# Optimization experiments

Measured on AMD Instinct MI355X. Metric: run time of the kernel, lower is better.

## Reference

```python
import jax, jax.numpy as jnp
import numpy as np

N_NODES = 100000
N_EDGES = 1600000
D_IN = 256
D_OUT = 256


def setup_inputs() -> dict:
    key = jax.random.key(0)
    ks = jax.random.split(key, 6)
    x_src = jax.random.normal(ks[0], (N_NODES, D_IN), dtype=jnp.float32)
    x_tgt = jax.random.normal(ks[1], (N_NODES, D_IN), dtype=jnp.float32)
    edge_index = jax.random.randint(ks[2], (2, N_EDGES), 0, N_NODES, dtype=jnp.int64)
    # torch Linear stores weight [out, in]; we store transposed [in, out] (same math)
    W_l = jax.random.normal(ks[3], (D_IN, D_OUT), dtype=jnp.float32) / np.sqrt(D_IN)
    b_l = jax.random.normal(ks[4], (D_OUT,), dtype=jnp.float32) * 0.01
    W_r = jax.random.normal(ks[5], (D_IN, D_OUT), dtype=jnp.float32) / np.sqrt(D_IN)
    return {"x_src": x_src, "x_tgt": x_tgt, "edge_index": edge_index,
            "W_l": W_l, "b_l": b_l, "W_r": W_r}


def reference(x_src, x_tgt, edge_index, W_l, b_l, W_r):
    row, col = edge_index[0], edge_index[1]
    n_tgt = x_tgt.shape[0]
    # gather source features along edges, scatter-mean into target nodes
    msgs = x_src[row]                                               # [E, D_IN]
    sums = jax.ops.segment_sum(msgs, col, num_segments=n_tgt)        # [N_tgt, D_IN]
    cnt = jax.ops.segment_sum(jnp.ones((row.shape[0],), x_src.dtype), col,
                              num_segments=n_tgt)                    # [N_tgt]
    aggr = sums / jnp.maximum(cnt, 1.0)[:, None]                     # mean; empty segs -> 0
    return aggr @ W_l + b_l + x_tgt @ W_r
```

## Files before the change

### kernel.cpp

```cpp
#include <hip/hip_runtime.h>
#include <hip/hip_bf16.h>

#define D 256
#define BW 128
#define CH 16384
#define SBCAP 2560

typedef __attribute__((ext_vector_type(8))) short short8;
typedef __attribute__((ext_vector_type(4))) float floatx4;
typedef __attribute__((ext_vector_type(4))) int intx4;

static __device__ __forceinline__ unsigned short f2bf(float f) {
  unsigned int u = __builtin_bit_cast(unsigned int, f);
  u += 0x7FFFu + ((u >> 16) & 1u);
  return (unsigned short)(u >> 16);
}

static __device__ __forceinline__ void gld_lds16(const unsigned short* g, unsigned short* l) {
  __builtin_amdgcn_global_load_lds(
      (const __attribute__((address_space(1))) unsigned int*)g,
      (__attribute__((address_space(3))) unsigned int*)l, 16, 0, 0);
}

static __device__ __forceinline__ int detect_is64(const int* ei32, int* sflag) {
  if (threadIdx.x < 64) {
    int v = ei32[2 * threadIdx.x + 1];
    unsigned long long nz = __ballot(v != 0);
    if (threadIdx.x == 0) *sflag = (nz == 0ULL) ? 1 : 0;
  }
  __syncthreads();
  return *sflag;
}

static __device__ __forceinline__ int edge_at(const void* ei, int is64, long long idx) {
  return is64 ? (int)((const long long*)ei)[idx] : ((const int*)ei)[idx];
}

__global__ __launch_bounds__(256) void scatter_kernel(const void* __restrict__ ei,
                                                      unsigned int* __restrict__ bucketbuf,
                                                      int* __restrict__ bcur,
                                                      int E, int N, int NBUCK) {
  __shared__ unsigned int recs[CH];
  __shared__ unsigned short bkt[CH];
  __shared__ unsigned short inv[CH];
  __shared__ int cnt[1025];
  __shared__ int lofs[1025];
  __shared__ int gb[1024];
  __shared__ int sflag;
  int t = threadIdx.x;
  long long base = (long long)blockIdx.x * CH;
  if (base >= E) return;
  int is64 = detect_is64((const int*)ei, &sflag);
  int count = (int)((E - base) < CH ? (E - base) : CH);

  for (int i = t; i <= NBUCK; i += 256) cnt[i] = 0;
  __syncthreads();

  for (int i = t; i < count; i += 256) {
    int c = edge_at(ei, is64, (long long)E + base + i);
    int s = edge_at(ei, is64, base + i);
    bool valid = (unsigned)c < (unsigned)N && (unsigned)s < (unsigned)N;
    int b = valid ? (c >> 7) : NBUCK;
    recs[i] = valid ? (((unsigned)s << 7) | (unsigned)(c & (BW - 1))) : 0u;
    bkt[i] = (unsigned short)b;
    atomicAdd(&cnt[b], 1);
  }
  __syncthreads();

  int i0 = t * 4;
  int v0 = (i0 + 0 <= NBUCK) ? cnt[i0 + 0] : 0;
  int v1 = (i0 + 1 <= NBUCK) ? cnt[i0 + 1] : 0;
  int v2 = (i0 + 2 <= NBUCK) ? cnt[i0 + 2] : 0;
  int v3 = (i0 + 3 <= NBUCK) ? cnt[i0 + 3] : 0;
  gb[t] = v0 + v1 + v2 + v3;
  __syncthreads();
  for (int d = 1; d < 256; d <<= 1) {
    int v = (t >= d) ? gb[t - d] : 0;
    __syncthreads();
    gb[t] += v;
    __syncthreads();
  }
  int excl = (t == 0) ? 0 : gb[t - 1];
  __syncthreads();
  if (i0 + 0 <= NBUCK) lofs[i0 + 0] = excl;
  if (i0 + 1 <= NBUCK) lofs[i0 + 1] = excl + v0;
  if (i0 + 2 <= NBUCK) lofs[i0 + 2] = excl + v0 + v1;
  if (i0 + 3 <= NBUCK) lofs[i0 + 3] = excl + v0 + v1 + v2;
  __syncthreads();

#pragma unroll
  for (int j = 0; j < 4; ++j) {
    int idx = i0 + j;
    if (idx < NBUCK) {
      int len = lofs[idx + 1] - lofs[idx];
      gb[idx] = (len > 0) ? atomicAdd(&bcur[idx], len) : 0;
    }
  }
  for (int i = t; i <= NBUCK; i += 256) cnt[i] = lofs[i];
  __syncthreads();

  for (int i = t; i < count; i += 256) {
    int p = atomicAdd(&cnt[bkt[i]], 1);
    inv[p] = (unsigned short)i;
  }
  __syncthreads();

  for (int p = t; p < count; p += 256) {
    int i = inv[p];
    int b = bkt[i];
    if (b < NBUCK) {
      int pos = gb[b] + (p - lofs[b]);
      if (pos < SBCAP) bucketbuf[(size_t)b * SBCAP + pos] = recs[i];
    }
  }
}

__global__ void bucket_scan_kernel(const int* __restrict__ bcur, int* __restrict__ bucket_base,
                                   int* __restrict__ offsets, int NBUCK, int N) {
  __shared__ int part[1024];
  int t = threadIdx.x;
  int tot = 0;
  if (t < NBUCK) {
    int v = bcur[t];
    tot = v > SBCAP ? SBCAP : v;
  }
  part[t] = tot;
  __syncthreads();
  for (int d = 1; d < 1024; d <<= 1) {
    int v = (t >= d) ? part[t - d] : 0;
    __syncthreads();
    part[t] += v;
    __syncthreads();
  }
  if (t < NBUCK) bucket_base[t] = part[t] - tot;
  if (t == NBUCK - 1) { bucket_base[NBUCK] = part[t]; offsets[N] = part[t]; }
}

__global__ __launch_bounds__(256) void bucket_csr_kernel(const unsigned int* __restrict__ bucketbuf,
                                                         const int* __restrict__ bcur,
                                                         const int* __restrict__ bucket_base,
                                                         int* __restrict__ offsets,
                                                         int* __restrict__ edge_src,
                                                         int NBUCK, int N) {
  __shared__ unsigned int recs[SBCAP];
  __shared__ int cnt[BW];
  __shared__ int scn[BW + 1];
  int b = blockIdx.x, t = threadIdx.x;
  int len = bcur[b]; if (len > SBCAP) len = SBCAP;
  if (t < BW) cnt[t] = 0;
  __syncthreads();
  for (int i = t; i < len; i += 256) {
    unsigned int r = bucketbuf[(size_t)b * SBCAP + i];
    recs[i] = r;
    atomicAdd(&cnt[r & (BW - 1)], 1);
  }
  __syncthreads();
  if (t == 0) {
    int run = 0;
    scn[0] = 0;
#pragma unroll
    for (int i = 0; i < BW; ++i) { run += cnt[i]; scn[i + 1] = run; }
  }
  __syncthreads();
  int gbase = bucket_base[b];
  if (t < BW) {
    int node = b * BW + t;
    if (node < N) offsets[node] = gbase + scn[t];
    cnt[t] = 0;
  }
  __syncthreads();
  for (int i = t; i < len; i += 256) {
    unsigned int r = recs[i];
    int tg = r & (BW - 1);
    int p = atomicAdd(&cnt[tg], 1);
    edge_src[gbase + scn[tg] + p] = (int)(r >> 7);
  }
}

__global__ void wtx_kernel(const float* __restrict__ Wl, const float* __restrict__ Wr,
                           unsigned short* __restrict__ Wt,
                           const float* __restrict__ x, unsigned int* __restrict__ xf8,
                           long long n16) {
  long long bid = blockIdx.x;
  int t = threadIdx.x;
  if (bid < 512) {
    int idx = (int)bid * 256 + t;
    int oc = idx >> 9, k = idx & 511;
    float v = (k < 256) ? Wl[k * 256 + oc] : Wr[(k - 256) * 256 + oc];
    Wt[idx] = f2bf(v);
  } else {
    long long i = (bid - 512) * 256 + t;
    if (i >= n16) return;
    const float* src = x + i * 16;
    intx4 w;
#pragma unroll
    for (int j = 0; j < 4; ++j) {
      floatx4 f = *(const floatx4*)(src + j * 4);
      int d = __builtin_amdgcn_cvt_pk_fp8_f32(f[0], f[1], 0, false);
      d = __builtin_amdgcn_cvt_pk_fp8_f32(f[2], f[3], d, true);
      w[j] = d;
    }
    *(intx4*)&xf8[i * 4] = w;
  }
}

__global__ __launch_bounds__(256) void aggr_f8_kernel(const unsigned int* __restrict__ xf8,
                                                      const int* __restrict__ offsets,
                                                      const int* __restrict__ edge_src,
                                                      unsigned short* __restrict__ aggr,
                                                      int n_tgt) {
  int node = blockIdx.x * 4 + (threadIdx.x >> 6);
  if (node >= n_tgt) return;
  int lane = threadIdx.x & 63;
  int q = lane >> 4;
  int fl = lane & 15;
  int start = offsets[node], end = offsets[node + 1];
  int deg = end - start;

  float a[16];
#pragma unroll
  for (int k = 0; k < 16; ++k) a[k] = 0.f;

  if (deg > 0) {
    int last = end - 1;
    for (int i = start + q; i < end; i += 16) {
      int e1 = i + 4, e2 = i + 8, e3 = i + 12;
      int s0 = edge_src[i];
      int s1 = edge_src[e1 < end ? e1 : last];
      int s2 = edge_src[e2 < end ? e2 : last];
      int s3 = edge_src[e3 < end ? e3 : last];
      float m1 = e1 < end ? 1.f : 0.f;
      float m2 = e2 < end ? 1.f : 0.f;
      float m3 = e3 < end ? 1.f : 0.f;
      intx4 w0 = *(const intx4*)&xf8[(size_t)s0 * 64 + fl * 4];
      intx4 w1 = *(const intx4*)&xf8[(size_t)s1 * 64 + fl * 4];
      intx4 w2 = *(const intx4*)&xf8[(size_t)s2 * 64 + fl * 4];
      intx4 w3 = *(const intx4*)&xf8[(size_t)s3 * 64 + fl * 4];
#pragma unroll
      for (int j = 0; j < 4; ++j) {
        {
          auto lo = __builtin_amdgcn_cvt_pk_f32_fp8(w0[j], false);
          auto hi = __builtin_amdgcn_cvt_pk_f32_fp8(w0[j], true);
          a[4 * j + 0] += lo[0]; a[4 * j + 1] += lo[1];
          a[4 * j + 2] += hi[0]; a[4 * j + 3] += hi[1];
        }
        {
          auto lo = __builtin_amdgcn_cvt_pk_f32_fp8(w1[j], false);
          auto hi = __builtin_amdgcn_cvt_pk_f32_fp8(w1[j], true);
          a[4 * j + 0] = fmaf(lo[0], m1, a[4 * j + 0]);
          a[4 * j + 1] = fmaf(lo[1], m1, a[4 * j + 1]);
          a[4 * j + 2] = fmaf(hi[0], m1, a[4 * j + 2]);
          a[4 * j + 3] = fmaf(hi[1], m1, a[4 * j + 3]);
        }
        {
          auto lo = __builtin_amdgcn_cvt_pk_f32_fp8(w2[j], false);
          auto hi = __builtin_amdgcn_cvt_pk_f32_fp8(w2[j], true);
          a[4 * j + 0] = fmaf(lo[0], m2, a[4 * j + 0]);
          a[4 * j + 1] = fmaf(lo[1], m2, a[4 * j + 1]);
          a[4 * j + 2] = fmaf(hi[0], m2, a[4 * j + 2]);
          a[4 * j + 3] = fmaf(hi[1], m2, a[4 * j + 3]);
        }
        {
          auto lo = __builtin_amdgcn_cvt_pk_f32_fp8(w3[j], false);
          auto hi = __builtin_amdgcn_cvt_pk_f32_fp8(w3[j], true);
          a[4 * j + 0] = fmaf(lo[0], m3, a[4 * j + 0]);
          a[4 * j + 1] = fmaf(lo[1], m3, a[4 * j + 1]);
          a[4 * j + 2] = fmaf(hi[0], m3, a[4 * j + 2]);
          a[4 * j + 3] = fmaf(hi[1], m3, a[4 * j + 3]);
        }
      }
    }
  }

#pragma unroll
  for (int k = 0; k < 16; ++k) {
    a[k] += __shfl_xor(a[k], 16);
    a[k] += __shfl_xor(a[k], 32);
  }

  if (lane < 16) {
    float inv = 1.f / (float)(deg > 0 ? deg : 1);
    short8 r0, r1;
#pragma unroll
    for (int k = 0; k < 8; ++k) {
      r0[k] = (short)f2bf(a[k] * inv);
      r1[k] = (short)f2bf(a[8 + k] * inv);
    }
    *(short8*)&aggr[(size_t)node * D + fl * 16] = r0;
    *(short8*)&aggr[(size_t)node * D + fl * 16 + 8] = r1;
  }
}

__global__ void aggr_f32_kernel(const float* __restrict__ xsrc, const int* __restrict__ offsets,
                                const int* __restrict__ edge_src, float* __restrict__ aggr) {
  int node = blockIdx.x;
  int t = threadIdx.x;
  int start = offsets[node], end = offsets[node + 1];
  float acc = 0.f;
  int i = start;
  for (; i + 4 <= end; i += 4) {
    int s0 = edge_src[i], s1 = edge_src[i + 1], s2 = edge_src[i + 2], s3 = edge_src[i + 3];
    acc += xsrc[(size_t)s0 * D + t];
    acc += xsrc[(size_t)s1 * D + t];
    acc += xsrc[(size_t)s2 * D + t];
    acc += xsrc[(size_t)s3 * D + t];
  }
  for (; i < end; ++i) acc += xsrc[(size_t)edge_src[i] * D + t];
  int deg = end - start;
  aggr[(size_t)node * D + t] = acc / (float)(deg > 0 ? deg : 1);
}

#define TSTRIDE 260
__global__ __launch_bounds__(512, 2) void gemm256_kernel(const unsigned short* __restrict__ aggr,
                                                         const float* __restrict__ xtgt,
                                                         const unsigned short* __restrict__ Wt,
                                                         const float* __restrict__ bias,
                                                         float* __restrict__ out, int n_tgt) {
  __shared__ __align__(16) union {
    struct { unsigned short A[2][16384]; unsigned short B[2][16384]; } s;
    float T[64 * TSTRIDE];
  } smem;
  int t = threadIdx.x;
  int lane = t & 63, wid = t >> 6;
  int lr = lane & 15, lq = lane >> 4;
  int wr = wid >> 2, wc = wid & 3;
  int mbase = blockIdx.x * 256;

  floatx4 acc[8][4];
#pragma unroll
  for (int mt = 0; mt < 8; ++mt)
#pragma unroll
    for (int nt = 0; nt < 4; ++nt) acc[mt][nt] = (floatx4){0.f, 0.f, 0.f, 0.f};

  floatx4 st[8];

  auto stageA_gld = [&](int c, int buf) {
    int kbase = c * 64;
#pragma unroll
    for (int r = 0; r < 4; ++r) {
      int s = wid * 256 + r * 64 + lane;
      int row = s >> 3, ch = s & 7;
      int grow = mbase + row; if (grow >= n_tgt) grow = n_tgt - 1;
      const unsigned short* src = aggr + (size_t)grow * 256 + kbase + ((ch ^ (row & 7)) * 8);
      gld_lds16(src, &smem.s.A[buf][(size_t)(wid * 256 + r * 64) * 8]);
    }
  };
  auto stageB_gld = [&](int c, int buf) {
    int kbase = c * 64;
#pragma unroll
    for (int r = 0; r < 4; ++r) {
      int s = wid * 256 + r * 64 + lane;
      int oc = s >> 3, ch = s & 7;
      const unsigned short* src = Wt + (size_t)oc * 512 + kbase + ((ch ^ (oc & 7)) * 8);
      gld_lds16(src, &smem.s.B[buf][(size_t)(wid * 256 + r * 64) * 8]);
    }
  };
  auto loadX = [&](int c) {
    int koff = c * 64 - 256;
#pragma unroll
    for (int r = 0; r < 4; ++r) {
      int s = r * 512 + t;
      int row = s >> 3, ch = s & 7;
      int grow = mbase + row; if (grow >= n_tgt) grow = n_tgt - 1;
      const float* src = xtgt + (size_t)grow * 256 + koff + ch * 8;
      st[2 * r]     = *(const floatx4*)src;
      st[2 * r + 1] = *(const floatx4*)(src + 4);
    }
  };
  auto writeX = [&](int buf) {
#pragma unroll
    for (int r = 0; r < 4; ++r) {
      int s = r * 512 + t;
      int row = s >> 3, ch = s & 7;
      short8 v;
      v[0] = (short)f2bf(st[2 * r][0]); v[1] = (short)f2bf(st[2 * r][1]);
      v[2] = (short)f2bf(st[2 * r][2]); v[3] = (short)f2bf(st[2 * r][3]);
      v[4] = (short)f2bf(st[2 * r + 1][0]); v[5] = (short)f2bf(st[2 * r + 1][1]);
      v[6] = (short)f2bf(st[2 * r + 1][2]); v[7] = (short)f2bf(st[2 * r + 1][3]);
      *(short8*)&smem.s.A[buf][(size_t)(row * 8 + (ch ^ (row & 7))) * 8] = v;
    }
  };
  auto compute = [&](int buf) {
#pragma unroll
    for (int ks2 = 0; ks2 < 2; ++ks2) {
      short8 b[4];
#pragma unroll
      for (int nt = 0; nt < 4; ++nt) {
        int oc = wc * 64 + nt * 16 + lr;
        int phys = (ks2 * 4 + lq) ^ (oc & 7);
        b[nt] = *(const short8*)&smem.s.B[buf][(size_t)(oc * 8 + phys) * 8];
      }
#pragma unroll
      for (int mt = 0; mt < 8; ++mt) {
        int row = wr * 128 + mt * 16 + lr;
        int phys = (ks2 * 4 + lq) ^ (row & 7);
        short8 a = *(const short8*)&smem.s.A[buf][(size_t)(row * 8 + phys) * 8];
#pragma unroll
        for (int nt = 0; nt < 4; ++nt)
          acc[mt][nt] = __builtin_amdgcn_mfma_f32_16x16x32_bf16(a, b[nt], acc[mt][nt], 0, 0, 0);
      }
    }
  };

  stageA_gld(0, 0);
  stageB_gld(0, 0);
  __syncthreads();

  int cur = 0;
#pragma unroll
  for (int c = 0; c < 8; ++c) {
    int nxt = cur ^ 1;
    if (c + 1 < 8) {
      stageB_gld(c + 1, nxt);
      if (c + 1 < 4) stageA_gld(c + 1, nxt);
      else loadX(c + 1);
    }
    compute(cur);
    if (c + 1 >= 4 && c + 1 < 8) writeX(nxt);
    __syncthreads();
    cur = nxt;
  }

  float bv[4];
#pragma unroll
  for (int nt = 0; nt < 4; ++nt) bv[nt] = bias[wc * 64 + nt * 16 + lr];

#pragma unroll
  for (int p = 0; p < 4; ++p) {
    if (wr == (p >> 1)) {
      int mtb = (p & 1) * 4;
#pragma unroll
      for (int mt2 = 0; mt2 < 4; ++mt2) {
        int mt = mtb + mt2;
#pragma unroll
        for (int nt = 0; nt < 4; ++nt) {
          int oc = wc * 64 + nt * 16 + lr;
#pragma unroll
          for (int r4 = 0; r4 < 4; ++r4) {
            int lrow = mt2 * 16 + lq * 4 + r4;
            smem.T[lrow * TSTRIDE + oc] = acc[mt][nt][r4] + bv[nt];
          }
        }
      }
    }
    __syncthreads();
#pragma unroll
    for (int u = 0; u < 8; ++u) {
      int idx = u * 512 + t;
      int row = idx >> 6, col4 = idx & 63;
      int node = mbase + p * 64 + row;
      if (node < n_tgt) {
        floatx4 v = *(const floatx4*)&smem.T[row * TSTRIDE + col4 * 4];
        *(floatx4*)&out[(size_t)node * D + col4 * 4] = v;
      }
    }
    __syncthreads();
  }
}

__global__ __launch_bounds__(256) void gemm_fb_kernel(const float* __restrict__ aggrp,
                                                      const float* __restrict__ xtgt,
                                                      const unsigned short* __restrict__ Wt,
                                                      const float* __restrict__ bias,
                                                      float* __restrict__ out, int n_tgt) {
  __shared__ __align__(16) unsigned short A_lds[64 * 256];
  int t = threadIdx.x;
  int mbase = blockIdx.x * 64;
  int lane = t & 63, w = t >> 6;
  int lr = lane & 15, lq = lane >> 4;

  floatx4 acc[4][4];
#pragma unroll
  for (int mt = 0; mt < 4; ++mt)
#pragma unroll
    for (int nt = 0; nt < 4; ++nt) acc[mt][nt] = (floatx4){0.f, 0.f, 0.f, 0.f};

  const unsigned short* WtW = Wt + ((size_t)(64 * w + lr)) * 512 + lq * 8;

  for (int ph = 0; ph < 2; ++ph) {
    const float* srcbase = ph == 0 ? aggrp : xtgt;
#pragma unroll
    for (int it = 0; it < 8; ++it) {
      int chunk = it * 256 + t;
      int r = chunk >> 5, c = chunk & 31;
      int node = mbase + r;
      floatx4 f0 = {0.f, 0.f, 0.f, 0.f}, f1 = {0.f, 0.f, 0.f, 0.f};
      if (node < n_tgt) {
        f0 = *(const floatx4*)&srcbase[(size_t)node * D + c * 8];
        f1 = *(const floatx4*)&srcbase[(size_t)node * D + c * 8 + 4];
      }
      short8 v;
      v[0] = (short)f2bf(f0[0]); v[1] = (short)f2bf(f0[1]);
      v[2] = (short)f2bf(f0[2]); v[3] = (short)f2bf(f0[3]);
      v[4] = (short)f2bf(f1[0]); v[5] = (short)f2bf(f1[1]);
      v[6] = (short)f2bf(f1[2]); v[7] = (short)f2bf(f1[3]);
      int sc = c ^ (r & 7);
      *(short8*)&A_lds[r * 256 + sc * 8] = v;
    }
    __syncthreads();
#pragma unroll
    for (int ks = 0; ks < 8; ++ks) {
      short8 a[4], b[4];
#pragma unroll
      for (int mt = 0; mt < 4; ++mt) {
        int row = 16 * mt + lr;
        int chunk = (ks * 4 + lq) ^ (row & 7);
        a[mt] = *(const short8*)&A_lds[row * 256 + chunk * 8];
      }
#pragma unroll
      for (int nt = 0; nt < 4; ++nt)
        b[nt] = *(const short8*)&WtW[(size_t)nt * 16 * 512 + (ph * 8 + ks) * 32];
#pragma unroll
      for (int mt = 0; mt < 4; ++mt)
#pragma unroll
        for (int nt = 0; nt < 4; ++nt)
          acc[mt][nt] = __builtin_amdgcn_mfma_f32_16x16x32_bf16(a[mt], b[nt], acc[mt][nt], 0, 0, 0);
    }
    __syncthreads();
  }

#pragma unroll
  for (int nt = 0; nt < 4; ++nt) {
    int oc = 64 * w + 16 * nt + lr;
    float bv = bias[oc];
#pragma unroll
    for (int mt = 0; mt < 4; ++mt) {
#pragma unroll
      for (int r4 = 0; r4 < 4; ++r4) {
        int node = mbase + 16 * mt + lq * 4 + r4;
        if (node < n_tgt) out[(size_t)node * D + oc] = acc[mt][nt][r4] + bv;
      }
    }
  }
}

extern "C" void kernel_launch(void* const* d_in, const int* in_sizes, int n_in,
                              void* d_out, int out_size, void* d_ws, size_t ws_size,
                              hipStream_t stream) {
  const float* x_src = (const float*)d_in[0];
  const float* x_tgt = (const float*)d_in[1];
  const void* ei = d_in[2];
  const float* W_l = (const float*)d_in[3];
  const float* b_l = (const float*)d_in[4];
  const float* W_r = (const float*)d_in[5];
  float* out = (float*)d_out;

  const int N_s = in_sizes[0] / D;
  const int N_t = in_sizes[1] / D;
  const int E = in_sizes[2] / 2;
  int NBUCK = (N_t + BW - 1) / BW;
  if (NBUCK > 1024) NBUCK = 1024;

  char* ws = (char*)d_ws;
  size_t o = 0;
  auto alloc = [&](size_t bytes) { size_t cur = o; o = (o + bytes + 255) & ~(size_t)255; return cur; };
  int* bcur              = (int*)(ws + alloc((size_t)NBUCK * 4));
  size_t zero_end        = o;
  unsigned int* bucketbuf = (unsigned int*)(ws + alloc((size_t)NBUCK * SBCAP * 4));
  int* bucket_base       = (int*)(ws + alloc(((size_t)NBUCK + 1) * 4));
  int* offsets           = (int*)(ws + alloc(((size_t)N_t + 1) * 4));
  int* edge_src          = (int*)(ws + alloc((size_t)E * 4));
  unsigned short* Wt     = (unsigned short*)(ws + alloc((size_t)256 * 512 * 2));
  unsigned int* xf8      = (unsigned int*)(ws + alloc((size_t)N_s * D));
  unsigned short* aggr_b = (unsigned short*)(ws + alloc((size_t)N_t * D * 2));
  size_t f8_end          = o;

  bool f8_path = (ws_size >= f8_end);

  hipMemsetAsync(ws, 0, zero_end, stream);

  int sb = (int)(((long long)E + CH - 1) / CH);
  scatter_kernel<<<sb, 256, 0, stream>>>(ei, bucketbuf, bcur, E, N_t, NBUCK);
  bucket_scan_kernel<<<1, 1024, 0, stream>>>(bcur, bucket_base, offsets, NBUCK, N_t);
  bucket_csr_kernel<<<NBUCK, 256, 0, stream>>>(bucketbuf, bcur, bucket_base, offsets,
                                               edge_src, NBUCK, N_t);

  if (f8_path) {
    long long n16 = (long long)N_s * D / 16;
    int xblocks = 512 + (int)((n16 + 255) / 256);
    wtx_kernel<<<xblocks, 256, 0, stream>>>(W_l, W_r, Wt, x_src, xf8, n16);
    aggr_f8_kernel<<<(N_t + 3) / 4, 256, 0, stream>>>(xf8, offsets, edge_src, aggr_b, N_t);
    gemm256_kernel<<<(N_t + 255) / 256, 512, 0, stream>>>(aggr_b, x_tgt, Wt, b_l, out, N_t);
  } else {
    wtx_kernel<<<512, 256, 0, stream>>>(W_l, W_r, Wt, x_src, xf8, 0);
    aggr_f32_kernel<<<N_t, 256, 0, stream>>>(x_src, offsets, edge_src, out);
    gemm_fb_kernel<<<(N_t + 63) / 64, 256, 0, stream>>>(out, x_tgt, Wt, b_l, out, N_t);
  }
}
```

Baseline: 236.0 us.

## Slice fp8 source features into 32-column tables and drop global bucket scan

```diff
diff --git a/kernel.cpp b/kernel.cpp
--- a/kernel.cpp
+++ b/kernel.cpp
@@ -5,8 +5,10 @@
 #define BW 128
 #define CH 16384
 #define SBCAP 2560
+#define NSLICE 8
 
 typedef __attribute__((ext_vector_type(8))) short short8;
+typedef __attribute__((ext_vector_type(4))) short short4v;
 typedef __attribute__((ext_vector_type(4))) float floatx4;
 typedef __attribute__((ext_vector_type(4))) int intx4;
 
@@ -115,31 +117,9 @@
   }
 }
 
-__global__ void bucket_scan_kernel(const int* __restrict__ bcur, int* __restrict__ bucket_base,
-                                   int* __restrict__ offsets, int NBUCK, int N) {
-  __shared__ int part[1024];
-  int t = threadIdx.x;
-  int tot = 0;
-  if (t < NBUCK) {
-    int v = bcur[t];
-    tot = v > SBCAP ? SBCAP : v;
-  }
-  part[t] = tot;
-  __syncthreads();
-  for (int d = 1; d < 1024; d <<= 1) {
-    int v = (t >= d) ? part[t - d] : 0;
-    __syncthreads();
-    part[t] += v;
-    __syncthreads();
-  }
-  if (t < NBUCK) bucket_base[t] = part[t] - tot;
-  if (t == NBUCK - 1) { bucket_base[NBUCK] = part[t]; offsets[N] = part[t]; }
-}
-
 __global__ __launch_bounds__(256) void bucket_csr_kernel(const unsigned int* __restrict__ bucketbuf,
                                                          const int* __restrict__ bcur,
-                                                         const int* __restrict__ bucket_base,
-                                                         int* __restrict__ offsets,
+                                                         int* __restrict__ offp,
                                                          int* __restrict__ edge_src,
                                                          int NBUCK, int N) {
   __shared__ unsigned int recs[SBCAP];
@@ -162,10 +142,14 @@
     for (int i = 0; i < BW; ++i) { run += cnt[i]; scn[i + 1] = run; }
   }
   __syncthreads();
-  int gbase = bucket_base[b];
+  int gbase = b * SBCAP;
   if (t < BW) {
     int node = b * BW + t;
-    if (node < N) offsets[node] = gbase + scn[t];
+    if (node < N) {
+      int deg = scn[t + 1] - scn[t];
+      if (deg > 2047) deg = 2047;
+      offp[node] = ((gbase + scn[t]) << 11) | deg;
+    }
     cnt[t] = 0;
   }
   __syncthreads();
@@ -179,8 +163,8 @@
 
 __global__ void wtx_kernel(const float* __restrict__ Wl, const float* __restrict__ Wr,
                            unsigned short* __restrict__ Wt,
-                           const float* __restrict__ x, unsigned int* __restrict__ xf8,
-                           long long n16) {
+                           const float* __restrict__ x, unsigned int* __restrict__ xf8s,
+                           int N) {
   long long bid = blockIdx.x;
   int t = threadIdx.x;
   if (bid < 512) {
@@ -190,128 +174,80 @@
     Wt[idx] = f2bf(v);
   } else {
     long long i = (bid - 512) * 256 + t;
-    if (i >= n16) return;
-    const float* src = x + i * 16;
-    intx4 w;
-#pragma unroll
-    for (int j = 0; j < 4; ++j) {
+    if (i >= (long long)NSLICE * N) return;
+    int s = (int)(i / N);
+    int n = (int)(i - (long long)s * N);
+    const float* src = x + (size_t)n * 256 + s * 32;
+    unsigned int w[8];
+#pragma unroll
+    for (int j = 0; j < 8; ++j) {
       floatx4 f = *(const floatx4*)(src + j * 4);
       int d = __builtin_amdgcn_cvt_pk_fp8_f32(f[0], f[1], 0, false);
       d = __builtin_amdgcn_cvt_pk_fp8_f32(f[2], f[3], d, true);
-      w[j] = d;
-    }
-    *(intx4*)&xf8[i * 4] = w;
-  }
-}
-
-__global__ __launch_bounds__(256) void aggr_f8_kernel(const unsigned int* __restrict__ xf8,
-                                                      const int* __restrict__ offsets,
-                                                      const int* __restrict__ edge_src,
-                                                      unsigned short* __restrict__ aggr,
-                                                      int n_tgt) {
-  int node = blockIdx.x * 4 + (threadIdx.x >> 6);
-  if (node >= n_tgt) return;
+      w[j] = (unsigned int)d;
+    }
+    unsigned int* dst = xf8s + (size_t)s * N * 8 + (size_t)n * 8;
+    *(intx4*)dst       = (intx4){(int)w[0], (int)w[1], (int)w[2], (int)w[3]};
+    *(intx4*)(dst + 4) = (intx4){(int)w[4], (int)w[5], (int)w[6], (int)w[7]};
+  }
+}
+
+__global__ __launch_bounds__(256) void aggr_slice_kernel(const unsigned int* __restrict__ xf8s,
+                                                         const int* __restrict__ offp,
+                                                         const int* __restrict__ edge_src,
+                                                         unsigned short* __restrict__ aggr_s,
+                                                         int N) {
+  int s = blockIdx.x & (NSLICE - 1);
+  int g = blockIdx.x >> 3;
+  int node = g * 4 + (threadIdx.x >> 6);
+  if (node >= N) return;
   int lane = threadIdx.x & 63;
-  int q = lane >> 4;
-  int fl = lane & 15;
-  int start = offsets[node], end = offsets[node + 1];
-  int deg = end - start;
-
-  float a[16];
-#pragma unroll
-  for (int k = 0; k < 16; ++k) a[k] = 0.f;
-
-  if (deg > 0) {
-    int last = end - 1;
-    for (int i = start + q; i < end; i += 16) {
-      int e1 = i + 4, e2 = i + 8, e3 = i + 12;
-      int s0 = edge_src[i];
-      int s1 = edge_src[e1 < end ? e1 : last];
-      int s2 = edge_src[e2 < end ? e2 : last];
-      int s3 = edge_src[e3 < end ? e3 : last];
-      float m1 = e1 < end ? 1.f : 0.f;
-      float m2 = e2 < end ? 1.f : 0.f;
-      float m3 = e3 < end ? 1.f : 0.f;
-      intx4 w0 = *(const intx4*)&xf8[(size_t)s0 * 64 + fl * 4];
-      intx4 w1 = *(const intx4*)&xf8[(size_t)s1 * 64 + fl * 4];
-      intx4 w2 = *(const intx4*)&xf8[(size_t)s2 * 64 + fl * 4];
-      intx4 w3 = *(const intx4*)&xf8[(size_t)s3 * 64 + fl * 4];
-#pragma unroll
-      for (int j = 0; j < 4; ++j) {
-        {
-          auto lo = __builtin_amdgcn_cvt_pk_f32_fp8(w0[j], false);
-          auto hi = __builtin_amdgcn_cvt_pk_f32_fp8(w0[j], true);
-          a[4 * j + 0] += lo[0]; a[4 * j + 1] += lo[1];
-          a[4 * j + 2] += hi[0]; a[4 * j + 3] += hi[1];
-        }
-        {
-          auto lo = __builtin_amdgcn_cvt_pk_f32_fp8(w1[j], false);
-          auto hi = __builtin_amdgcn_cvt_pk_f32_fp8(w1[j], true);
-          a[4 * j + 0] = fmaf(lo[0], m1, a[4 * j + 0]);
-          a[4 * j + 1] = fmaf(lo[1], m1, a[4 * j + 1]);
-          a[4 * j + 2] = fmaf(hi[0], m1, a[4 * j + 2]);
-          a[4 * j + 3] = fmaf(hi[1], m1, a[4 * j + 3]);
-        }
-        {
-          auto lo = __builtin_amdgcn_cvt_pk_f32_fp8(w2[j], false);
-          auto hi = __builtin_amdgcn_cvt_pk_f32_fp8(w2[j], true);
-          a[4 * j + 0] = fmaf(lo[0], m2, a[4 * j + 0]);
-          a[4 * j + 1] = fmaf(lo[1], m2, a[4 * j + 1]);
-          a[4 * j + 2] = fmaf(hi[0], m2, a[4 * j + 2]);
-          a[4 * j + 3] = fmaf(hi[1], m2, a[4 * j + 3]);
-        }
-        {
-          auto lo = __builtin_amdgcn_cvt_pk_f32_fp8(w3[j], false);
-          auto hi = __builtin_amdgcn_cvt_pk_f32_fp8(w3[j], true);
-          a[4 * j + 0] = fmaf(lo[0], m3, a[4 * j + 0]);
-          a[4 * j + 1] = fmaf(lo[1], m3, a[4 * j + 1]);
-          a[4 * j + 2] = fmaf(hi[0], m3, a[4 * j + 2]);
-          a[4 * j + 3] = fmaf(hi[1], m3, a[4 * j + 3]);
-        }
-      }
-    }
-  }
-
-#pragma unroll
-  for (int k = 0; k < 16; ++k) {
-    a[k] += __shfl_xor(a[k], 16);
-    a[k] += __shfl_xor(a[k], 32);
-  }
-
-  if (lane < 16) {
+  int e8 = lane >> 3, f = lane & 7;
+  int p = offp[node];
+  int start = ((unsigned)p) >> 11;
+  int deg = p & 2047;
+  int end = start + deg;
+
+  const unsigned int* tab = xf8s + (size_t)s * N * 8;
+  float a0 = 0.f, a1 = 0.f, a2 = 0.f, a3 = 0.f;
+  for (int i = start + e8; i < end; i += 8) {
+    int src = edge_src[i];
+    unsigned int w = tab[(size_t)src * 8 + f];
+    auto lo = __builtin_amdgcn_cvt_pk_f32_fp8(w, false);
+    auto hi = __builtin_amdgcn_cvt_pk_f32_fp8(w, true);
+    a0 += lo[0]; a1 += lo[1]; a2 += hi[0]; a3 += hi[1];
+  }
+#pragma unroll
+  for (int m = 8; m <= 32; m <<= 1) {
+    a0 += __shfl_xor(a0, m);
+    a1 += __shfl_xor(a1, m);
+    a2 += __shfl_xor(a2, m);
+    a3 += __shfl_xor(a3, m);
+  }
+  if (e8 == 0) {
     float inv = 1.f / (float)(deg > 0 ? deg : 1);
-    short8 r0, r1;
-#pragma unroll
-    for (int k = 0; k < 8; ++k) {
-      r0[k] = (short)f2bf(a[k] * inv);
-      r1[k] = (short)f2bf(a[8 + k] * inv);
-    }
-    *(short8*)&aggr[(size_t)node * D + fl * 16] = r0;
-    *(short8*)&aggr[(size_t)node * D + fl * 16 + 8] = r1;
-  }
-}
-
-__global__ void aggr_f32_kernel(const float* __restrict__ xsrc, const int* __restrict__ offsets,
+    short4v r;
+    r[0] = (short)f2bf(a0 * inv); r[1] = (short)f2bf(a1 * inv);
+    r[2] = (short)f2bf(a2 * inv); r[3] = (short)f2bf(a3 * inv);
+    *(short4v*)&aggr_s[(size_t)s * N * 32 + (size_t)node * 32 + f * 4] = r;
+  }
+}
+
+__global__ void aggr_f32_kernel(const float* __restrict__ xsrc, const int* __restrict__ offp,
                                 const int* __restrict__ edge_src, float* __restrict__ aggr) {
   int node = blockIdx.x;
   int t = threadIdx.x;
-  int start = offsets[node], end = offsets[node + 1];
+  int p = offp[node];
+  int start = ((unsigned)p) >> 11;
+  int deg = p & 2047;
+  int end = start + deg;
   float acc = 0.f;
-  int i = start;
-  for (; i + 4 <= end; i += 4) {
-    int s0 = edge_src[i], s1 = edge_src[i + 1], s2 = edge_src[i + 2], s3 = edge_src[i + 3];
-    acc += xsrc[(size_t)s0 * D + t];
-    acc += xsrc[(size_t)s1 * D + t];
-    acc += xsrc[(size_t)s2 * D + t];
-    acc += xsrc[(size_t)s3 * D + t];
-  }
-  for (; i < end; ++i) acc += xsrc[(size_t)edge_src[i] * D + t];
-  int deg = end - start;
+  for (int i = start; i < end; ++i) acc += xsrc[(size_t)edge_src[i] * D + t];
   aggr[(size_t)node * D + t] = acc / (float)(deg > 0 ? deg : 1);
 }
 
 #define TSTRIDE 260
-__global__ __launch_bounds__(512, 2) void gemm256_kernel(const unsigned short* __restrict__ aggr,
+__global__ __launch_bounds__(512, 2) void gemm256_kernel(const unsigned short* __restrict__ aggr_s,
                                                          const float* __restrict__ xtgt,
                                                          const unsigned short* __restrict__ Wt,
                                                          const float* __restrict__ bias,
@@ -341,7 +277,9 @@
       int s = wid * 256 + r * 64 + lane;
       int row = s >> 3, ch = s & 7;
       int grow = mbase + row; if (grow >= n_tgt) grow = n_tgt - 1;
-      const unsigned short* src = aggr + (size_t)grow * 256 + kbase + ((ch ^ (row & 7)) * 8);
+      int kk = kbase + ((ch ^ (row & 7)) * 8);
+      int sl = kk >> 5, off = kk & 31;
+      const unsigned short* src = aggr_s + (size_t)sl * n_tgt * 32 + (size_t)grow * 32 + off;
       gld_lds16(src, &smem.s.A[buf][(size_t)(wid * 256 + r * 64) * 8]);
     }
   };
@@ -557,33 +495,30 @@
   int* bcur              = (int*)(ws + alloc((size_t)NBUCK * 4));
   size_t zero_end        = o;
   unsigned int* bucketbuf = (unsigned int*)(ws + alloc((size_t)NBUCK * SBCAP * 4));
-  int* bucket_base       = (int*)(ws + alloc(((size_t)NBUCK + 1) * 4));
-  int* offsets           = (int*)(ws + alloc(((size_t)N_t + 1) * 4));
-  int* edge_src          = (int*)(ws + alloc((size_t)E * 4));
+  int* offp              = (int*)(ws + alloc((size_t)N_t * 4));
+  int* edge_src          = (int*)(ws + alloc((size_t)NBUCK * SBCAP * 4));
   unsigned short* Wt     = (unsigned short*)(ws + alloc((size_t)256 * 512 * 2));
-  unsigned int* xf8      = (unsigned int*)(ws + alloc((size_t)N_s * D));
-  unsigned short* aggr_b = (unsigned short*)(ws + alloc((size_t)N_t * D * 2));
+  unsigned int* xf8s     = (unsigned int*)(ws + alloc((size_t)N_s * D));
+  unsigned short* aggr_s = (unsigned short*)(ws + alloc((size_t)N_t * D * 2));
   size_t f8_end          = o;
 
-  bool f8_path = (ws_size >= f8_end);
+  bool f8_path = (ws_size >= f8_end) && (N_s == N_t);
 
   hipMemsetAsync(ws, 0, zero_end, stream);
 
   int sb = (int)(((long long)E + CH - 1) / CH);
   scatter_kernel<<<sb, 256, 0, stream>>>(ei, bucketbuf, bcur, E, N_t, NBUCK);
-  bucket_scan_kernel<<<1, 1024, 0, stream>>>(bcur, bucket_base, offsets, NBUCK, N_t);
-  bucket_csr_kernel<<<NBUCK, 256, 0, stream>>>(bucketbuf, bcur, bucket_base, offsets,
-                                               edge_src, NBUCK, N_t);
+  bucket_csr_kernel<<<NBUCK, 256, 0, stream>>>(bucketbuf, bcur, offp, edge_src, NBUCK, N_t);
 
   if (f8_path) {
-    long long n16 = (long long)N_s * D / 16;
-    int xblocks = 512 + (int)((n16 + 255) / 256);
-    wtx_kernel<<<xblocks, 256, 0, stream>>>(W_l, W_r, Wt, x_src, xf8, n16);
-    aggr_f8_kernel<<<(N_t + 3) / 4, 256, 0, stream>>>(xf8, offsets, edge_src, aggr_b, N_t);
-    gemm256_kernel<<<(N_t + 255) / 256, 512, 0, stream>>>(aggr_b, x_tgt, Wt, b_l, out, N_t);
+    int xblocks = 512 + (int)(((long long)NSLICE * N_s + 255) / 256);
+    wtx_kernel<<<xblocks, 256, 0, stream>>>(W_l, W_r, Wt, x_src, xf8s, N_s);
+    aggr_slice_kernel<<<((N_t + 3) / 4) * NSLICE, 256, 0, stream>>>(xf8s, offp, edge_src,
+                                                                    aggr_s, N_t);
+    gemm256_kernel<<<(N_t + 255) / 256, 512, 0, stream>>>(aggr_s, x_tgt, Wt, b_l, out, N_t);
   } else {
-    wtx_kernel<<<512, 256, 0, stream>>>(W_l, W_r, Wt, x_src, xf8, 0);
-    aggr_f32_kernel<<<N_t, 256, 0, stream>>>(x_src, offsets, edge_src, out);
+    wtx_kernel<<<512, 256, 0, stream>>>(W_l, W_r, Wt, x_src, xf8s, 0);
+    aggr_f32_kernel<<<N_t, 256, 0, stream>>>(x_src, offp, edge_src, out);
     gemm_fb_kernel<<<(N_t + 63) / 64, 256, 0, stream>>>(out, x_tgt, Wt, b_l, out, N_t);
   }
 }
```

After: 383.4 us. 1.62x slower.

## Drop bucket scan and memset by using fixed-stride CSR with packed offset/degree

Applied to the files above, without the earlier changes.

```diff
diff --git a/kernel.cpp b/kernel.cpp
--- a/kernel.cpp
+++ b/kernel.cpp
@@ -115,31 +115,9 @@
   }
 }
 
-__global__ void bucket_scan_kernel(const int* __restrict__ bcur, int* __restrict__ bucket_base,
-                                   int* __restrict__ offsets, int NBUCK, int N) {
-  __shared__ int part[1024];
-  int t = threadIdx.x;
-  int tot = 0;
-  if (t < NBUCK) {
-    int v = bcur[t];
-    tot = v > SBCAP ? SBCAP : v;
-  }
-  part[t] = tot;
-  __syncthreads();
-  for (int d = 1; d < 1024; d <<= 1) {
-    int v = (t >= d) ? part[t - d] : 0;
-    __syncthreads();
-    part[t] += v;
-    __syncthreads();
-  }
-  if (t < NBUCK) bucket_base[t] = part[t] - tot;
-  if (t == NBUCK - 1) { bucket_base[NBUCK] = part[t]; offsets[N] = part[t]; }
-}
-
 __global__ __launch_bounds__(256) void bucket_csr_kernel(const unsigned int* __restrict__ bucketbuf,
                                                          const int* __restrict__ bcur,
-                                                         const int* __restrict__ bucket_base,
-                                                         int* __restrict__ offsets,
+                                                         int* __restrict__ offp,
                                                          int* __restrict__ edge_src,
                                                          int NBUCK, int N) {
   __shared__ unsigned int recs[SBCAP];
@@ -162,10 +140,14 @@
     for (int i = 0; i < BW; ++i) { run += cnt[i]; scn[i + 1] = run; }
   }
   __syncthreads();
-  int gbase = bucket_base[b];
+  int gbase = b * SBCAP;
   if (t < BW) {
     int node = b * BW + t;
-    if (node < N) offsets[node] = gbase + scn[t];
+    if (node < N) {
+      int deg = scn[t + 1] - scn[t];
+      if (deg > 2047) deg = 2047;
+      offp[node] = (int)((((unsigned)(gbase + scn[t])) << 11) | (unsigned)deg);
+    }
     cnt[t] = 0;
   }
   __syncthreads();
@@ -180,9 +162,12 @@
 __global__ void wtx_kernel(const float* __restrict__ Wl, const float* __restrict__ Wr,
                            unsigned short* __restrict__ Wt,
                            const float* __restrict__ x, unsigned int* __restrict__ xf8,
-                           long long n16) {
+                           long long n16, int* __restrict__ bcur, int NBUCK) {
   long long bid = blockIdx.x;
   int t = threadIdx.x;
+  if (bid == 0) {
+    for (int i = t; i < NBUCK; i += 256) bcur[i] = 0;
+  }
   if (bid < 512) {
     int idx = (int)bid * 256 + t;
     int oc = idx >> 9, k = idx & 511;
@@ -205,7 +190,7 @@
 }
 
 __global__ __launch_bounds__(256) void aggr_f8_kernel(const unsigned int* __restrict__ xf8,
-                                                      const int* __restrict__ offsets,
+                                                      const int* __restrict__ offp,
                                                       const int* __restrict__ edge_src,
                                                       unsigned short* __restrict__ aggr,
                                                       int n_tgt) {
@@ -214,8 +199,10 @@
   int lane = threadIdx.x & 63;
   int q = lane >> 4;
   int fl = lane & 15;
-  int start = offsets[node], end = offsets[node + 1];
-  int deg = end - start;
+  int pk = offp[node];
+  int start = (int)(((unsigned)pk) >> 11);
+  int deg = pk & 2047;
+  int end = start + deg;
 
   float a[16];
 #pragma unroll
@@ -291,22 +278,16 @@
   }
 }
 
-__global__ void aggr_f32_kernel(const float* __restrict__ xsrc, const int* __restrict__ offsets,
+__global__ void aggr_f32_kernel(const float* __restrict__ xsrc, const int* __restrict__ offp,
                                 const int* __restrict__ edge_src, float* __restrict__ aggr) {
   int node = blockIdx.x;
   int t = threadIdx.x;
-  int start = offsets[node], end = offsets[node + 1];
+  int pk = offp[node];
+  int start = (int)(((unsigned)pk) >> 11);
+  int deg = pk & 2047;
+  int end = start + deg;
   float acc = 0.f;
-  int i = start;
-  for (; i + 4 <= end; i += 4) {
-    int s0 = edge_src[i], s1 = edge_src[i + 1], s2 = edge_src[i + 2], s3 = edge_src[i + 3];
-    acc += xsrc[(size_t)s0 * D + t];
-    acc += xsrc[(size_t)s1 * D + t];
-    acc += xsrc[(size_t)s2 * D + t];
-    acc += xsrc[(size_t)s3 * D + t];
-  }
-  for (; i < end; ++i) acc += xsrc[(size_t)edge_src[i] * D + t];
-  int deg = end - start;
+  for (int i = start; i < end; ++i) acc += xsrc[(size_t)edge_src[i] * D + t];
   aggr[(size_t)node * D + t] = acc / (float)(deg > 0 ? deg : 1);
 }
 
@@ -555,11 +536,9 @@
   size_t o = 0;
   auto alloc = [&](size_t bytes) { size_t cur = o; o = (o + bytes + 255) & ~(size_t)255; return cur; };
   int* bcur              = (int*)(ws + alloc((size_t)NBUCK * 4));
-  size_t zero_end        = o;
   unsigned int* bucketbuf = (unsigned int*)(ws + alloc((size_t)NBUCK * SBCAP * 4));
-  int* bucket_base       = (int*)(ws + alloc(((size_t)NBUCK + 1) * 4));
-  int* offsets           = (int*)(ws + alloc(((size_t)N_t + 1) * 4));
-  int* edge_src          = (int*)(ws + alloc((size_t)E * 4));
+  int* offp              = (int*)(ws + alloc((size_t)N_t * 4));
+  int* edge_src          = (int*)(ws + alloc((size_t)NBUCK * SBCAP * 4));
   unsigned short* Wt     = (unsigned short*)(ws + alloc((size_t)256 * 512 * 2));
   unsigned int* xf8      = (unsigned int*)(ws + alloc((size_t)N_s * D));
   unsigned short* aggr_b = (unsigned short*)(ws + alloc((size_t)N_t * D * 2));
@@ -567,23 +546,19 @@
 
   bool f8_path = (ws_size >= f8_end);
 
-  hipMemsetAsync(ws, 0, zero_end, stream);
+  long long n16 = f8_path ? (long long)N_s * D / 16 : 0;
+  int xblocks = 512 + (int)((n16 + 255) / 256);
+  wtx_kernel<<<xblocks, 256, 0, stream>>>(W_l, W_r, Wt, x_src, xf8, n16, bcur, NBUCK);
 
   int sb = (int)(((long long)E + CH - 1) / CH);
   scatter_kernel<<<sb, 256, 0, stream>>>(ei, bucketbuf, bcur, E, N_t, NBUCK);
-  bucket_scan_kernel<<<1, 1024, 0, stream>>>(bcur, bucket_base, offsets, NBUCK, N_t);
-  bucket_csr_kernel<<<NBUCK, 256, 0, stream>>>(bucketbuf, bcur, bucket_base, offsets,
-                                               edge_src, NBUCK, N_t);
+  bucket_csr_kernel<<<NBUCK, 256, 0, stream>>>(bucketbuf, bcur, offp, edge_src, NBUCK, N_t);
 
   if (f8_path) {
-    long long n16 = (long long)N_s * D / 16;
-    int xblocks = 512 + (int)((n16 + 255) / 256);
-    wtx_kernel<<<xblocks, 256, 0, stream>>>(W_l, W_r, Wt, x_src, xf8, n16);
-    aggr_f8_kernel<<<(N_t + 3) / 4, 256, 0, stream>>>(xf8, offsets, edge_src, aggr_b, N_t);
+    aggr_f8_kernel<<<(N_t + 3) / 4, 256, 0, stream>>>(xf8, offp, edge_src, aggr_b, N_t);
     gemm256_kernel<<<(N_t + 255) / 256, 512, 0, stream>>>(aggr_b, x_tgt, Wt, b_l, out, N_t);
   } else {
-    wtx_kernel<<<512, 256, 0, stream>>>(W_l, W_r, Wt, x_src, xf8, 0);
-    aggr_f32_kernel<<<N_t, 256, 0, stream>>>(x_src, offsets, edge_src, out);
+    aggr_f32_kernel<<<N_t, 256, 0, stream>>>(x_src, offp, edge_src, out);
     gemm_fb_kernel<<<(N_t + 63) / 64, 256, 0, stream>>>(out, x_tgt, Wt, b_l, out, N_t);
   }
 }
```

New measurement: 221.6 us. -6.1%, faster.
